# Kernel optimization log

Measured on AMD Instinct MI355X. Metric: run time of the kernel, lower is better.

Reference implementation:

```python
import jax, jax.numpy as jnp
import numpy as np

C = 128          # channel_size
H = 2            # num_head
HD = C // H      # per-head dim = 64
SCALE = C ** 0.5 # note: module scales by sqrt(channel_size), not sqrt(head_dim)


def setup_inputs() -> dict:
    key = jax.random.key(0)
    k_x, k_w, k_b = jax.random.split(key, 3)
    x = jax.random.normal(k_x, (8, 64, 256, C), dtype=jnp.float32)
    # nn.Linear(C, 3C): weight [3C, C], bias [3C]; y = x @ W.T + b
    bound = 1.0 / np.sqrt(C)
    W_qkv = jax.random.uniform(k_w, (3 * C, C), dtype=jnp.float32, minval=-bound, maxval=bound)
    b_qkv = jax.random.uniform(k_b, (3 * C,), dtype=jnp.float32, minval=-bound, maxval=bound)
    return {"x": x, "W_qkv": W_qkv, "b_qkv": b_qkv}


def reference(x, W_qkv, b_qkv):
    b, l, g, _ = x.shape
    qkv = jnp.einsum('blgc,dc->blgd', x, W_qkv) + b_qkv        # [b,l,g,3C]
    # rearrange 'b l g (d h c) -> d b l h g c'
    qkv = qkv.reshape(b, l, g, 3, H, HD)
    qkv = jnp.transpose(qkv, (3, 0, 1, 4, 2, 5))               # [3,b,l,h,g,c]
    q, k, v = qkv[0], qkv[1], qkv[2]
    score = jnp.einsum('blhgc,blhkc->blhgk', q, k) / SCALE      # [b,l,h,g,g]
    score = jax.nn.softmax(score, axis=-1)
    out = jnp.einsum('blhgk,blhkc->blhgc', score, v)            # [b,l,h,g,c]
    # rearrange 'b l h g c -> b l g (h c)'
    out = jnp.transpose(out, (0, 1, 3, 2, 4)).reshape(b, l, g, H * HD)
    return out
```

## Files before the change

kernel.cpp:

```cpp
#include <hip/hip_runtime.h>
#include <hip/hip_bf16.h>


typedef __bf16 bf16x8 __attribute__((ext_vector_type(8)));
typedef float  f32x4  __attribute__((ext_vector_type(4)));

#define MFMA16(a, b, c) __builtin_amdgcn_mfma_f32_16x16x32_bf16((a), (b), (c), 0, 0, 0)

namespace dmsa {

constexpr int G  = 256;
constexpr int C  = 128;
constexpr int HD = 64;
constexpr float QSCALE = 1.4426950408889634f * 0.08838834764831845f;

__device__ __forceinline__ unsigned pack2(float a, float b) {
    union { __hip_bfloat162 h; unsigned u; } c;
    c.h = __float22bfloat162_rn(make_float2(a, b));
    return c.u;
}
__device__ __forceinline__ uint2 pack4(float a, float b, float c, float d) {
    uint2 r; r.x = pack2(a, b); r.y = pack2(c, d); return r;
}
__device__ __forceinline__ uint4 pack8(const float* p) {
    uint4 r;
    r.x = pack2(p[0], p[1]); r.y = pack2(p[2], p[3]);
    r.z = pack2(p[4], p[5]); r.w = pack2(p[6], p[7]);
    return r;
}
__device__ __forceinline__ bf16x8 lds8(const ushort* p) { return *(const bf16x8*)p; }
__device__ __forceinline__ bf16x8 ldg8(const ushort* p) { return *(const bf16x8*)p; }

__global__ void convw(const float* __restrict__ W, ushort* __restrict__ wbf) {
    int t = blockIdx.x * 256 + threadIdx.x;
    float tmp[8];
    const float* p = W + (size_t)t * 8;
    *(float4*)tmp       = *(const float4*)p;
    *(float4*)(tmp + 4) = *(const float4*)(p + 4);
    *(uint4*)(wbf + (size_t)t * 8) = pack8(tmp);
}

__global__ __launch_bounds__(256)
void prep(const float* __restrict__ x, const ushort* __restrict__ wbf,
          const float* __restrict__ bias, ushort* __restrict__ qb,
          ushort* __restrict__ kb, ushort* __restrict__ vt)
{
    __shared__ ushort xa[64 * 136];
    __shared__ ushort wb[128 * 136];

    const int tid = threadIdx.x, wv = tid >> 6, lane = tid & 63;
    const int l16 = lane & 15, quad = lane >> 4;
    const int mt = blockIdx.x, bl = mt >> 2, g0 = (mt & 3) * 64;

    const float* xg = x + (size_t)mt * 64 * C;
    #pragma unroll
    for (int i = 0; i < 4; ++i) {
        int e = (tid + 256 * i) * 8, r = e >> 7, c = e & 127;
        float tmp[8];
        *(float4*)tmp       = *(const float4*)(xg + r * C + c);
        *(float4*)(tmp + 4) = *(const float4*)(xg + r * C + c + 4);
        *(uint4*)(xa + r * 136 + c) = pack8(tmp);
    }

    for (int nt = 0; nt < 3; ++nt) {
        __syncthreads();
        const ushort* wg = wbf + (size_t)nt * 128 * C;
        #pragma unroll
        for (int i = 0; i < 8; ++i) {
            int e = (tid + 256 * i) * 8, r = e >> 7, c = e & 127;
            *(uint4*)(wb + r * 136 + c) = *(const uint4*)(wg + r * C + c);
        }
        __syncthreads();

        const f32x4 z4 = {0.f, 0.f, 0.f, 0.f};
        if (nt < 2) {
            f32x4 acc[8];
            #pragma unroll
            for (int m = 0; m < 8; ++m) acc[m] = z4;
            #pragma unroll
            for (int kk = 0; kk < 4; ++kk) {
                bf16x8 b = lds8(xa + (wv * 16 + l16) * 136 + kk * 32 + quad * 8);
                #pragma unroll
                for (int m = 0; m < 8; ++m) {
                    bf16x8 a = lds8(wb + (m * 16 + l16) * 136 + kk * 32 + quad * 8);
                    acc[m] = MFMA16(a, b, acc[m]);
                }
            }
            const float scale = (nt == 0) ? QSCALE : 1.0f;
            ushort* dst0 = (nt == 0) ? qb : kb;
            const int g = g0 + wv * 16 + l16;
            #pragma unroll
            for (int m = 0; m < 8; ++m) {
                int ch = m * 16 + quad * 4;
                float4 bs = *(const float4*)(bias + nt * C + ch);
                int h = ch >> 6, cp = ch & 63;
                ushort* d = dst0 + (((size_t)(bl * 2 + h)) * G + g) * HD + cp;
                *(uint2*)d = pack4((acc[m][0] + bs.x) * scale,
                                   (acc[m][1] + bs.y) * scale,
                                   (acc[m][2] + bs.z) * scale,
                                   (acc[m][3] + bs.w) * scale);
            }
        } else {
            f32x4 acc[4][2];
            #pragma unroll
            for (int m = 0; m < 4; ++m)
                #pragma unroll
                for (int n = 0; n < 2; ++n) acc[m][n] = z4;
            #pragma unroll
            for (int kk = 0; kk < 4; ++kk) {
                bf16x8 a[4], b[2];
                #pragma unroll
                for (int m = 0; m < 4; ++m)
                    a[m] = lds8(xa + (m * 16 + l16) * 136 + kk * 32 + quad * 8);
                #pragma unroll
                for (int n = 0; n < 2; ++n)
                    b[n] = lds8(wb + (wv * 32 + n * 16 + l16) * 136 + kk * 32 + quad * 8);
                #pragma unroll
                for (int m = 0; m < 4; ++m)
                    #pragma unroll
                    for (int n = 0; n < 2; ++n)
                        acc[m][n] = MFMA16(a[m], b[n], acc[m][n]);
            }
            const int h = wv >> 1;
            #pragma unroll
            for (int n = 0; n < 2; ++n) {
                int ch = wv * 32 + n * 16 + l16;
                float bv = bias[2 * C + ch];
                int cp = ch & 63;
                #pragma unroll
                for (int m = 0; m < 4; ++m) {
                    int g = g0 + m * 16 + quad * 4;
                    ushort* d = vt + (((size_t)(bl * 2 + h)) * HD + cp) * G + g;
                    *(uint2*)d = pack4(acc[m][n][0] + bv, acc[m][n][1] + bv,
                                       acc[m][n][2] + bv, acc[m][n][3] + bv);
                }
            }
        }
    }
}

__global__ __launch_bounds__(256)
void attn(const ushort* __restrict__ qb, const ushort* __restrict__ kb,
          const ushort* __restrict__ vt, float* __restrict__ out)
{
    __shared__ ushort pt[4 * 64 * 40];

    const int tid = threadIdx.x, wv = tid >> 6, lane = tid & 63;
    const int l16 = lane & 15, quad = lane >> 4;
    const int bl = blockIdx.x, h = blockIdx.y;

    const size_t blh = (size_t)(bl * 2 + h);
    const ushort* q = qb + blh * G * HD;
    const ushort* k = kb + blh * G * HD;
    const ushort* v = vt + blh * HD * G;
    ushort* ptw = pt + wv * (64 * 40);

    bf16x8 qf[4][2];
    #pragma unroll
    for (int ni = 0; ni < 4; ++ni)
        #pragma unroll
        for (int kk = 0; kk < 2; ++kk)
            qf[ni][kk] = ldg8(q + (size_t)(wv * 64 + ni * 16 + l16) * HD
                              + kk * 32 + quad * 8);

    const f32x4 z4 = {0.f, 0.f, 0.f, 0.f};
    float lacc[4] = {0.f, 0.f, 0.f, 0.f};
    f32x4 oacc[4][4];
    #pragma unroll
    for (int mi = 0; mi < 4; ++mi)
        #pragma unroll
        for (int ni = 0; ni < 4; ++ni) oacc[mi][ni] = z4;

    for (int jt = 0; jt < 8; ++jt) {
        f32x4 s[2][4];
        #pragma unroll
        for (int mi = 0; mi < 2; ++mi)
            #pragma unroll
            for (int ni = 0; ni < 4; ++ni) s[mi][ni] = z4;

        #pragma unroll
        for (int kk = 0; kk < 2; ++kk) {
            bf16x8 kf[2];
            #pragma unroll
            for (int mi = 0; mi < 2; ++mi)
                kf[mi] = ldg8(k + (size_t)(jt * 32 + mi * 16 + l16) * HD
                              + kk * 32 + quad * 8);
            #pragma unroll
            for (int mi = 0; mi < 2; ++mi)
                #pragma unroll
                for (int ni = 0; ni < 4; ++ni)
                    s[mi][ni] = MFMA16(kf[mi], qf[ni][kk], s[mi][ni]);
        }

        #pragma unroll
        for (int mi = 0; mi < 2; ++mi)
            #pragma unroll
            for (int ni = 0; ni < 4; ++ni) {
                #pragma unroll
                for (int r = 0; r < 4; ++r) {
                    float p = exp2f(s[mi][ni][r]);
                    s[mi][ni][r] = p;
                    lacc[ni] += p;
                }
                *(uint2*)(ptw + (ni * 16 + l16) * 40 + mi * 16 + quad * 4) =
                    pack4(s[mi][ni][0], s[mi][ni][1], s[mi][ni][2], s[mi][ni][3]);
            }

        bf16x8 pf[4], vf[4];
        #pragma unroll
        for (int ni = 0; ni < 4; ++ni)
            pf[ni] = lds8(ptw + (ni * 16 + l16) * 40 + quad * 8);
        #pragma unroll
        for (int mi = 0; mi < 4; ++mi)
            vf[mi] = ldg8(v + (size_t)(mi * 16 + l16) * G + jt * 32 + quad * 8);
        #pragma unroll
        for (int mi = 0; mi < 4; ++mi)
            #pragma unroll
            for (int ni = 0; ni < 4; ++ni)
                oacc[mi][ni] = MFMA16(vf[mi], pf[ni], oacc[mi][ni]);
    }

    float* og = out + (size_t)bl * G * C + h * HD;
    #pragma unroll
    for (int ni = 0; ni < 4; ++ni) {
        float l = lacc[ni];
        l += __shfl_xor(l, 16);
        l += __shfl_xor(l, 32);
        float inv = 1.0f / l;
        int g = wv * 64 + ni * 16 + l16;
        #pragma unroll
        for (int mi = 0; mi < 4; ++mi) {
            float4 st;
            st.x = oacc[mi][ni][0] * inv; st.y = oacc[mi][ni][1] * inv;
            st.z = oacc[mi][ni][2] * inv; st.w = oacc[mi][ni][3] * inv;
            *(float4*)(og + (size_t)g * C + mi * 16 + quad * 4) = st;
        }
    }
}

}

extern "C" void kernel_launch(void* const* d_in, const int* in_sizes, int n_in,
                              void* d_out, int out_size, void* d_ws, size_t ws_size,
                              hipStream_t stream) {
    (void)in_sizes; (void)n_in; (void)out_size;

    const size_t SEG = (size_t)1024 * 256 * 64;
    if (ws_size < 3 * SEG * 2) return;

    const float* x    = (const float*)d_in[0];
    const float* W    = (const float*)d_in[1];
    const float* bias = (const float*)d_in[2];
    float* out = (float*)d_out;

    ushort* qb = (ushort*)d_ws;
    ushort* kb = qb + SEG;
    ushort* vt = kb + SEG;
    ushort* wbf = (ushort*)((char*)d_out + ((size_t)16777216 * 4 - 131072));

    dmsa::convw<<<dim3(24), dim3(256), 0, stream>>>(W, wbf);
    dmsa::prep<<<dim3(2048), dim3(256), 0, stream>>>(x, wbf, bias, qb, kb, vt);
    dmsa::attn<<<dim3(512, 2), dim3(256), 0, stream>>>(qb, kb, vt, out);
}
```

Measured before the change: 195.0 us.

## Stage QKV stores through LDS and double-buffer K/V tiles in attention

The projection kernel now writes its bf16 Q/K/V results into shared memory first, then copies them out as coalesced 16-byte row stores, replacing scattered 8-byte global writes. The V-transposed layout is also built in LDS before the store. The attention kernel stops having each wave read K and V fragments from global memory on its own. It cooperatively loads 64-token K/V chunks into double-buffered LDS, prefetching the next chunk into registers while computing on the current one. This cuts redundant global traffic across the four waves, at the cost of extra LDS usage and barriers that may reduce occupancy.

```diff
diff --git a/kernel.cpp b/kernel.cpp
--- a/kernel.cpp
+++ b/kernel.cpp
@@ -86,19 +86,30 @@
                     acc[m] = MFMA16(a, b, acc[m]);
                 }
             }
+            __syncthreads();
+
             const float scale = (nt == 0) ? QSCALE : 1.0f;
-            ushort* dst0 = (nt == 0) ? qb : kb;
-            const int g = g0 + wv * 16 + l16;
             #pragma unroll
             for (int m = 0; m < 8; ++m) {
                 int ch = m * 16 + quad * 4;
                 float4 bs = *(const float4*)(bias + nt * C + ch);
-                int h = ch >> 6, cp = ch & 63;
-                ushort* d = dst0 + (((size_t)(bl * 2 + h)) * G + g) * HD + cp;
-                *(uint2*)d = pack4((acc[m][0] + bs.x) * scale,
-                                   (acc[m][1] + bs.y) * scale,
-                                   (acc[m][2] + bs.z) * scale,
-                                   (acc[m][3] + bs.w) * scale);
+                *(uint2*)(wb + (wv * 16 + l16) * 136 + ch) =
+                    pack4((acc[m][0] + bs.x) * scale, (acc[m][1] + bs.y) * scale,
+                          (acc[m][2] + bs.z) * scale, (acc[m][3] + bs.w) * scale);
+            }
+            __syncthreads();
+
+            ushort* dst0 = (nt == 0) ? qb : kb;
+            #pragma unroll
+            for (int h = 0; h < 2; ++h) {
+                ushort* dsth = dst0 + ((size_t)(bl * 2 + h) * G + g0) * HD;
+                #pragma unroll
+                for (int j = 0; j < 2; ++j) {
+                    int f = tid + 256 * j;
+                    int tok = f >> 3, cc = (f & 7) * 8;
+                    *(uint4*)(dsth + tok * HD + cc) =
+                        *(const uint4*)(wb + tok * 136 + h * 64 + cc);
+                }
             }
         } else {
             f32x4 acc[4][2];
@@ -121,19 +132,29 @@
                     for (int n = 0; n < 2; ++n)
                         acc[m][n] = MFMA16(a[m], b[n], acc[m][n]);
             }
-            const int h = wv >> 1;
+            __syncthreads();
+
             #pragma unroll
             for (int n = 0; n < 2; ++n) {
                 int ch = wv * 32 + n * 16 + l16;
                 float bv = bias[2 * C + ch];
-                int cp = ch & 63;
                 #pragma unroll
                 for (int m = 0; m < 4; ++m) {
-                    int g = g0 + m * 16 + quad * 4;
-                    ushort* d = vt + (((size_t)(bl * 2 + h)) * HD + cp) * G + g;
-                    *(uint2*)d = pack4(acc[m][n][0] + bv, acc[m][n][1] + bv,
-                                       acc[m][n][2] + bv, acc[m][n][3] + bv);
+                    int tokb = m * 16 + quad * 4;
+                    *(uint2*)(wb + ch * 136 + tokb) =
+                        pack4(acc[m][n][0] + bv, acc[m][n][1] + bv,
+                              acc[m][n][2] + bv, acc[m][n][3] + bv);
                 }
+            }
+            __syncthreads();
+
+            #pragma unroll
+            for (int j = 0; j < 4; ++j) {
+                int f = tid + 256 * j;
+                int ch = f >> 3, gg = (f & 7) * 8;
+                int h = ch >> 6, cp = ch & 63;
+                *(uint4*)(vt + ((size_t)(bl * 2 + h) * HD + cp) * G + g0 + gg) =
+                    *(const uint4*)(wb + ch * 136 + gg);
             }
         }
     }
@@ -143,6 +164,8 @@
 void attn(const ushort* __restrict__ qb, const ushort* __restrict__ kb,
           const ushort* __restrict__ vt, float* __restrict__ out)
 {
+    __shared__ ushort kc[2][64 * 72];
+    __shared__ ushort vc[2][64 * 72];
     __shared__ ushort pt[4 * 64 * 40];
 
     const int tid = threadIdx.x, wv = tid >> 6, lane = tid & 63;
@@ -163,6 +186,21 @@
             qf[ni][kk] = ldg8(q + (size_t)(wv * 64 + ni * 16 + l16) * HD
                               + kk * 32 + quad * 8);
 
+    uint4 kr[2], vr[2];
+    #pragma unroll
+    for (int j = 0; j < 2; ++j) {
+        int f = tid + 256 * j;
+        kr[j] = *(const uint4*)(k + f * 8);
+        vr[j] = *(const uint4*)(v + (f >> 3) * G + (f & 7) * 8);
+    }
+    #pragma unroll
+    for (int j = 0; j < 2; ++j) {
+        int f = tid + 256 * j, row = f >> 3, cc = (f & 7) * 8;
+        *(uint4*)(&kc[0][row * 72 + cc]) = kr[j];
+        *(uint4*)(&vc[0][row * 72 + cc]) = vr[j];
+    }
+    __syncthreads();
+
     const f32x4 z4 = {0.f, 0.f, 0.f, 0.f};
     float lacc[4] = {0.f, 0.f, 0.f, 0.f};
     f32x4 oacc[4][4];
@@ -171,53 +209,76 @@
         #pragma unroll
         for (int ni = 0; ni < 4; ++ni) oacc[mi][ni] = z4;
 
-    for (int jt = 0; jt < 8; ++jt) {
-        f32x4 s[2][4];
-        #pragma unroll
-        for (int mi = 0; mi < 2; ++mi)
-            #pragma unroll
-            for (int ni = 0; ni < 4; ++ni) s[mi][ni] = z4;
-
-        #pragma unroll
-        for (int kk = 0; kk < 2; ++kk) {
-            bf16x8 kf[2];
+    for (int c = 0; c < 4; ++c) {
+        const int buf = c & 1;
+        if (c < 3) {
+            #pragma unroll
+            for (int j = 0; j < 2; ++j) {
+                int f = tid + 256 * j;
+                kr[j] = *(const uint4*)(k + (c + 1) * 64 * HD + f * 8);
+                vr[j] = *(const uint4*)(v + (f >> 3) * G + (c + 1) * 64 + (f & 7) * 8);
+            }
+        }
+
+        #pragma unroll
+        for (int sub = 0; sub < 2; ++sub) {
+            f32x4 s[2][4];
             #pragma unroll
             for (int mi = 0; mi < 2; ++mi)
-                kf[mi] = ldg8(k + (size_t)(jt * 32 + mi * 16 + l16) * HD
-                              + kk * 32 + quad * 8);
+                #pragma unroll
+                for (int ni = 0; ni < 4; ++ni) s[mi][ni] = z4;
+
+            #pragma unroll
+            for (int kk = 0; kk < 2; ++kk) {
+                bf16x8 kf[2];
+                #pragma unroll
+                for (int mi = 0; mi < 2; ++mi)
+                    kf[mi] = lds8(&kc[buf][(sub * 32 + mi * 16 + l16) * 72
+                                           + kk * 32 + quad * 8]);
+                #pragma unroll
+                for (int mi = 0; mi < 2; ++mi)
+                    #pragma unroll
+                    for (int ni = 0; ni < 4; ++ni)
+                        s[mi][ni] = MFMA16(kf[mi], qf[ni][kk], s[mi][ni]);
+            }
+
             #pragma unroll
             for (int mi = 0; mi < 2; ++mi)
                 #pragma unroll
+                for (int ni = 0; ni < 4; ++ni) {
+                    #pragma unroll
+                    for (int r = 0; r < 4; ++r) {
+                        float p = exp2f(s[mi][ni][r]);
+                        s[mi][ni][r] = p;
+                        lacc[ni] += p;
+                    }
+                    *(uint2*)(ptw + (ni * 16 + l16) * 40 + mi * 16 + quad * 4) =
+                        pack4(s[mi][ni][0], s[mi][ni][1], s[mi][ni][2], s[mi][ni][3]);
+                }
+
+            bf16x8 pf[4], vf[4];
+            #pragma unroll
+            for (int ni = 0; ni < 4; ++ni)
+                pf[ni] = lds8(ptw + (ni * 16 + l16) * 40 + quad * 8);
+            #pragma unroll
+            for (int mi = 0; mi < 4; ++mi)
+                vf[mi] = lds8(&vc[buf][(mi * 16 + l16) * 72 + sub * 32 + quad * 8]);
+            #pragma unroll
+            for (int mi = 0; mi < 4; ++mi)
+                #pragma unroll
                 for (int ni = 0; ni < 4; ++ni)
-                    s[mi][ni] = MFMA16(kf[mi], qf[ni][kk], s[mi][ni]);
-        }
-
-        #pragma unroll
-        for (int mi = 0; mi < 2; ++mi)
-            #pragma unroll
-            for (int ni = 0; ni < 4; ++ni) {
-                #pragma unroll
-                for (int r = 0; r < 4; ++r) {
-                    float p = exp2f(s[mi][ni][r]);
-                    s[mi][ni][r] = p;
-                    lacc[ni] += p;
-                }
-                *(uint2*)(ptw + (ni * 16 + l16) * 40 + mi * 16 + quad * 4) =
-                    pack4(s[mi][ni][0], s[mi][ni][1], s[mi][ni][2], s[mi][ni][3]);
-            }
-
-        bf16x8 pf[4], vf[4];
-        #pragma unroll
-        for (int ni = 0; ni < 4; ++ni)
-            pf[ni] = lds8(ptw + (ni * 16 + l16) * 40 + quad * 8);
-        #pragma unroll
-        for (int mi = 0; mi < 4; ++mi)
-            vf[mi] = ldg8(v + (size_t)(mi * 16 + l16) * G + jt * 32 + quad * 8);
-        #pragma unroll
-        for (int mi = 0; mi < 4; ++mi)
-            #pragma unroll
-            for (int ni = 0; ni < 4; ++ni)
-                oacc[mi][ni] = MFMA16(vf[mi], pf[ni], oacc[mi][ni]);
+                    oacc[mi][ni] = MFMA16(vf[mi], pf[ni], oacc[mi][ni]);
+        }
+
+        if (c < 3) {
+            #pragma unroll
+            for (int j = 0; j < 2; ++j) {
+                int f = tid + 256 * j, row = f >> 3, cc = (f & 7) * 8;
+                *(uint4*)(&kc[buf ^ 1][row * 72 + cc]) = kr[j];
+                *(uint4*)(&vc[buf ^ 1][row * 72 + cc]) = vr[j];
+            }
+        }
+        __syncthreads();
     }
 
     float* og = out + (size_t)bl * G * C + h * HD;
```

Result: no change. 192.5 us (-1.3%).
